# Kernel tuning notes

Hardware: AMD Instinct MI355X
Metric: run time of the kernel (lower is better)

Reference implementation:

```python
import jax, jax.numpy as jnp
import numpy as np

B, S, D = 8, 2048, 256
H = 4
DH = D // H  # 64


def setup_inputs() -> dict:
    key = jax.random.key(0)
    ks = jax.random.split(key, 6)
    x = jax.random.normal(ks[0], (B, S, D), dtype=jnp.float32)
    # Linear weights stored as (d_in, d_out) so y = x @ W (+ b)
    scale = 1.0 / np.sqrt(D)
    w_q = jax.random.normal(ks[1], (D, D), dtype=jnp.float32) * scale
    w_k = jax.random.normal(ks[2], (D, D), dtype=jnp.float32) * scale
    w_v = jax.random.normal(ks[3], (D, D), dtype=jnp.float32) * scale
    w_o = jax.random.normal(ks[4], (D, D), dtype=jnp.float32) * scale
    b_o = jax.random.normal(ks[5], (D,), dtype=jnp.float32) * 0.01
    return {"x": x, "w_q": w_q, "w_k": w_k, "w_v": w_v, "w_o": w_o, "b_o": b_o}


def reference(x, w_q, w_k, w_v, w_o, b_o):
    b, s, _ = x.shape
    # project and split heads: [b, h, s, dh]
    q = (x @ w_q).reshape(b, s, H, DH).transpose(0, 2, 1, 3)
    k = (x @ w_k).reshape(b, s, H, DH).transpose(0, 2, 1, 3)
    v = (x @ w_v).reshape(b, s, H, DH).transpose(0, 2, 1, 3)
    # full attention matrix [b, h, s, s] (matches original non-fused math)
    scores = jnp.einsum('bhqd,bhkd->bhqk', q, k) / jnp.sqrt(jnp.float32(DH))
    attn = jax.nn.softmax(scores, axis=-1)  # dropout is identity in eval
    ctx = jnp.einsum('bhqk,bhkd->bhqd', attn, v)
    ctx = ctx.transpose(0, 2, 1, 3).reshape(b, s, H * DH)
    return ctx @ w_o + b_o
```

## Files before the change

kernel.cpp:

```cpp
#include <hip/hip_runtime.h>
#include <hip/hip_fp16.h>
#include <math.h>

typedef _Float16 f16;
typedef _Float16 f16x8 __attribute__((ext_vector_type(8)));
typedef float f32x4 __attribute__((ext_vector_type(4)));

#define BB 8
#define SS 2048
#define DD 256
#define HH 4
#define DHH 64

#define LOG2E 1.44269504088896340736f
#define MOFF (4.0f * LOG2E)

__global__ __launch_bounds__(256) void prep_kernel(
    const float* __restrict__ wq, const float* __restrict__ wk,
    const float* __restrict__ wv, const float* __restrict__ wo,
    f16* __restrict__ wqkvT, f16* __restrict__ woT) {
  __shared__ f16 lds[64][72];
  int dout0 = blockIdx.x * 64;
  int k0 = blockIdx.y * 64;
  const float* src;
  f16* dst;
  int col0, drow;
  if (dout0 < 256)      { src = wq; dst = wqkvT; col0 = dout0;       drow = dout0; }
  else if (dout0 < 512) { src = wk; dst = wqkvT; col0 = dout0 - 256; drow = dout0; }
  else if (dout0 < 768) { src = wv; dst = wqkvT; col0 = dout0 - 512; drow = dout0; }
  else                  { src = wo; dst = woT;   col0 = dout0 - 768; drow = dout0 - 768; }

  int dl = threadIdx.x & 63, kl = threadIdx.x >> 6;
#pragma unroll
  for (int i = 0; i < 16; i++) {
    int kloc = i * 4 + kl;
    lds[kloc][dl] = (f16)src[(size_t)(k0 + kloc) * 256 + col0 + dl];
  }
  __syncthreads();
  int row_l = threadIdx.x >> 2, kq = threadIdx.x & 3;
  f16x8 v0, v1;
#pragma unroll
  for (int j = 0; j < 8; j++) v0[j] = lds[kq * 16 + j][row_l];
#pragma unroll
  for (int j = 0; j < 8; j++) v1[j] = lds[kq * 16 + 8 + j][row_l];
  f16* p = dst + (size_t)(drow + row_l) * 256 + k0 + kq * 16;
  *(f16x8*)p = v0;
  *(f16x8*)(p + 8) = v1;
}

__global__ __launch_bounds__(256) void qkv_gemm(
    const float* __restrict__ x, const f16* __restrict__ wT,
    f16* __restrict__ Q, f16* __restrict__ K, f16* __restrict__ VT) {
  __shared__ __attribute__((aligned(16))) f16 bstage[8][4][64][8];
  __shared__ __attribute__((aligned(16))) f16 lds_t[64][72];
  int m0 = blockIdx.x * 64;
  int which = blockIdx.y;
  int nbase = which * 256;
  int wave = threadIdx.x >> 6, lane = threadIdx.x & 63;
  int lm = lane & 15, quad = lane >> 4;

  const float* arow = x + (size_t)(m0 + wave * 16 + lm) * 256 + quad * 8;
  f16x8 a[8];
#pragma unroll
  for (int kk = 0; kk < 8; kk++) {
    f32x4 a0 = *(const f32x4*)(arow + kk * 32);
    f32x4 a1 = *(const f32x4*)(arow + kk * 32 + 4);
#pragma unroll
    for (int j = 0; j < 4; j++) { a[kk][j] = (f16)a0[j]; a[kk][j + 4] = (f16)a1[j]; }
  }

  f16x8 breg[8];
  auto bload = [&](int n0) {
#pragma unroll
    for (int kk = 0; kk < 8; kk++)
      breg[kk] = *(const f16x8*)(wT + (size_t)(n0 + wave * 16 + lm) * 256 + kk * 32 + quad * 8);
  };
  bload(nbase);

  int bb = m0 >> 11, s0 = m0 & 2047;
  for (int i = 0; i < 4; i++) {
    int n0 = nbase + i * 64;
#pragma unroll
    for (int kk = 0; kk < 8; kk++)
      *(f16x8*)&bstage[kk][wave][lane][0] = breg[kk];
    __syncthreads();
    if (i + 1 < 4) bload(nbase + (i + 1) * 64);

    f32x4 acc[4] = {};
#pragma unroll
    for (int kk = 0; kk < 8; kk++)
#pragma unroll
      for (int nt = 0; nt < 4; nt++) {
        f16x8 b = *(const f16x8*)&bstage[kk][nt][lane][0];
        acc[nt] = __builtin_amdgcn_mfma_f32_16x16x32_f16(a[kk], b, acc[nt], 0, 0, 0);
      }

    if (which < 2) {
      f16* dst = (which == 0) ? Q : K;
      int nb = n0 & 255;
#pragma unroll
      for (int nt = 0; nt < 4; nt++) {
        int dout = nb + nt * 16 + lm;
        int h = dout >> 6, dh = dout & 63;
#pragma unroll
        for (int r = 0; r < 4; r++) {
          int s = s0 + wave * 16 + quad * 4 + r;
          dst[(((size_t)(bb * HH + h) * SS + s) << 6) + dh] = (f16)acc[nt][r];
        }
      }
    } else {
      int h = i;
#pragma unroll
      for (int nt = 0; nt < 4; nt++)
#pragma unroll
        for (int r = 0; r < 4; r++)
          lds_t[nt * 16 + lm][wave * 16 + quad * 4 + r] = (f16)acc[nt][r];
      __syncthreads();
      int rr = threadIdx.x >> 2, cc = threadIdx.x & 3;
      f16* vrow = VT + ((size_t)(bb * HH + h) * DHH + rr) * SS + s0;
      f16x8 v0 = *(const f16x8*)&lds_t[rr][cc * 16];
      f16x8 v1 = *(const f16x8*)&lds_t[rr][cc * 16 + 8];
      *(f16x8*)(vrow + cc * 16) = v0;
      *(f16x8*)(vrow + cc * 16 + 8) = v1;
    }
    __syncthreads();
  }
}

__global__ __launch_bounds__(512) void attn_kernel(
    const f16* __restrict__ Q, const f16* __restrict__ K,
    const f16* __restrict__ VT, f16* __restrict__ ctx) {
  __shared__ __attribute__((aligned(16))) f16 kbuf[2][8][64][8];
  __shared__ __attribute__((aligned(16))) f16 vbuf[2][8][64][8];
  __shared__ __attribute__((aligned(16))) f16 lds_p[8][16][72];

  int qb = blockIdx.x, h = blockIdx.y, b = blockIdx.z;
  int wave = threadIdx.x >> 6, lane = threadIdx.x & 63;
  int lm = lane & 15, quad = lane >> 4;
  const f16* Qbh = Q + (size_t)(b * HH + h) * SS * DHH;
  const f16* Kbh = K + (size_t)(b * HH + h) * SS * DHH;
  const f16* Vbh = VT + (size_t)(b * HH + h) * DHH * SS;
  int q0 = qb * 128 + wave * 16;

  int kpf = wave >> 2, ntf = wave & 3;
  f16x8 tk, tv;
  auto stage_load = [&](int key0) {
    tk = *(const f16x8*)(Kbh + (key0 + ntf * 16 + lm) * DHH + kpf * 32 + quad * 8);
    tv = *(const f16x8*)(Vbh + (ntf * 16 + lm) * SS + key0 + kpf * 32 + quad * 8);
  };
  auto stage_write = [&](int buf) {
    *(f16x8*)&kbuf[buf][wave][lane][0] = tk;
    *(f16x8*)&vbuf[buf][wave][lane][0] = tv;
  };

  f16x8 aq[2];
#pragma unroll
  for (int kp = 0; kp < 2; kp++) {
    aq[kp] = *(const f16x8*)(Qbh + (q0 + lm) * DHH + kp * 32 + quad * 8);
#pragma unroll
    for (int j = 0; j < 8; j++) aq[kp][j] *= (f16)0.125f;
  }
  f16x8 vones;
#pragma unroll
  for (int j = 0; j < 8; j++) vones[j] = (f16)1.0f;

  f32x4 accO[4] = {};
  f32x4 accL = {};

  stage_load(0);
  stage_write(0);
  stage_load(64);

  const int NT = SS / 64;
  for (int t = 0; t < NT; t++) {
    int cur = t & 1;
    __syncthreads();

    if (t + 1 < NT) {
      stage_write(cur ^ 1);
      if (t + 2 < NT) stage_load((t + 2) * 64);
    }

    f32x4 accS[4] = {};
#pragma unroll
    for (int kp = 0; kp < 2; kp++)
#pragma unroll
      for (int nt = 0; nt < 4; nt++) {
        f16x8 bk = *(const f16x8*)&kbuf[cur][kp * 4 + nt][lane][0];
        accS[nt] = __builtin_amdgcn_mfma_f32_16x16x32_f16(aq[kp], bk, accS[nt], 0, 0, 0);
      }

#pragma unroll
    for (int nt = 0; nt < 4; nt++)
#pragma unroll
      for (int r = 0; r < 4; r++) {
        float p = __builtin_amdgcn_exp2f(__builtin_fmaf(accS[nt][r], LOG2E, -MOFF));
        lds_p[wave][quad * 4 + r][nt * 16 + lm] = (f16)p;
      }

#pragma unroll
    for (int kp = 0; kp < 2; kp++) {
      f16x8 ap = *(const f16x8*)&lds_p[wave][lm][kp * 32 + quad * 8];
      accL = __builtin_amdgcn_mfma_f32_16x16x32_f16(ap, vones, accL, 0, 0, 0);
#pragma unroll
      for (int nt = 0; nt < 4; nt++) {
        f16x8 bv = *(const f16x8*)&vbuf[cur][kp * 4 + nt][lane][0];
        accO[nt] = __builtin_amdgcn_mfma_f32_16x16x32_f16(ap, bv, accO[nt], 0, 0, 0);
      }
    }
  }

  float rinv[4];
#pragma unroll
  for (int r = 0; r < 4; r++) rinv[r] = 1.0f / accL[r];
#pragma unroll
  for (int nt = 0; nt < 4; nt++)
#pragma unroll
    for (int r = 0; r < 4; r++) {
      int s = q0 + quad * 4 + r;
      ctx[(size_t)(b * SS + s) * DD + h * DHH + nt * 16 + lm] =
          (f16)(accO[nt][r] * rinv[r]);
    }
}

__global__ __launch_bounds__(256) void out_gemm(
    const f16* __restrict__ ctxh, const f16* __restrict__ woT,
    const float* __restrict__ bo, float* __restrict__ out) {
  __shared__ __attribute__((aligned(16))) f16 bstage[8][4][64][8];
  int m0 = blockIdx.x * 64;
  int nbase = blockIdx.y * 128;
  int wave = threadIdx.x >> 6, lane = threadIdx.x & 63;
  int lm = lane & 15, quad = lane >> 4;
  const f16* arow = ctxh + (size_t)(m0 + wave * 16 + lm) * 256 + quad * 8;
  f16x8 a[8];
#pragma unroll
  for (int kk = 0; kk < 8; kk++) a[kk] = *(const f16x8*)(arow + kk * 32);

  f16x8 breg[8];
  auto bload = [&](int n0) {
#pragma unroll
    for (int kk = 0; kk < 8; kk++)
      breg[kk] = *(const f16x8*)(woT + (size_t)(n0 + wave * 16 + lm) * 256 + kk * 32 + quad * 8);
  };
  bload(nbase);

  for (int i = 0; i < 2; i++) {
    int n0 = nbase + i * 64;
#pragma unroll
    for (int kk = 0; kk < 8; kk++)
      *(f16x8*)&bstage[kk][wave][lane][0] = breg[kk];
    __syncthreads();
    if (i + 1 < 2) bload(nbase + 64);

    f32x4 acc[4] = {};
#pragma unroll
    for (int kk = 0; kk < 8; kk++)
#pragma unroll
      for (int nt = 0; nt < 4; nt++) {
        f16x8 bfr = *(const f16x8*)&bstage[kk][nt][lane][0];
        acc[nt] = __builtin_amdgcn_mfma_f32_16x16x32_f16(a[kk], bfr, acc[nt], 0, 0, 0);
      }
#pragma unroll
    for (int nt = 0; nt < 4; nt++) {
      int dout = n0 + nt * 16 + lm;
      float bias = bo[dout];
#pragma unroll
      for (int r = 0; r < 4; r++) {
        int t = m0 + wave * 16 + quad * 4 + r;
        out[(size_t)t * 256 + dout] = acc[nt][r] + bias;
      }
    }
    __syncthreads();
  }
}

extern "C" void kernel_launch(void* const* d_in, const int* in_sizes, int n_in,
                              void* d_out, int out_size, void* d_ws, size_t ws_size,
                              hipStream_t stream) {
  const float* x  = (const float*)d_in[0];
  const float* wq = (const float*)d_in[1];
  const float* wk = (const float*)d_in[2];
  const float* wv = (const float*)d_in[3];
  const float* wo = (const float*)d_in[4];
  const float* bo = (const float*)d_in[5];
  float* out = (float*)d_out;

  char* ws = (char*)d_ws;
  const size_t SZ = 8388608;
  f16* Qb    = (f16*)(ws);
  f16* Kb    = (f16*)(ws + SZ);
  f16* VTb   = (f16*)(ws + 2 * SZ);
  f16* ctxh  = (f16*)(ws + 3 * SZ);
  f16* wqkvT = (f16*)(ws + 4 * SZ);
  f16* woT   = (f16*)(ws + 4 * SZ + 393216);

  hipLaunchKernelGGL(prep_kernel, dim3(16, 4), dim3(256), 0, stream,
                     wq, wk, wv, wo, wqkvT, woT);
  hipLaunchKernelGGL(qkv_gemm, dim3(256, 3), dim3(256), 0, stream,
                     x, wqkvT, Qb, Kb, VTb);
  hipLaunchKernelGGL(attn_kernel, dim3(16, 4, 8), dim3(512), 0, stream,
                     Qb, Kb, VTb, ctxh);
  hipLaunchKernelGGL(out_gemm, dim3(256, 2), dim3(256), 0, stream,
                     ctxh, woT, bo, out);
}
```

Measured before the change: 160.6 us.

## Switch attention kernel to 32x32x16 MFMA with 32-row query tiles per wave

Rewrites the attention inner loop to use 32x32x16 f16 MFMA instructions. Each wave now owns 32 query rows, so a block has 4 waves (256 threads) covering the same 128 queries. Each thread stages two K and two V fragments per tile, and the P tile in LDS is reshaped to 32 rows. The larger MFMA shape should raise math per LDS read of K/V and cut the instruction count. In exchange it uses more accumulator registers per thread and has fewer waves per block to hide latency.

```diff
diff --git a/kernel.cpp b/kernel.cpp
--- a/kernel.cpp
+++ b/kernel.cpp
@@ -5,6 +5,7 @@
 typedef _Float16 f16;
 typedef _Float16 f16x8 __attribute__((ext_vector_type(8)));
 typedef float f32x4 __attribute__((ext_vector_type(4)));
+typedef float f32x16 __attribute__((ext_vector_type(16)));
 
 #define BB 8
 #define SS 2048
@@ -127,45 +128,49 @@
   }
 }
 
-__global__ __launch_bounds__(512) void attn_kernel(
+__global__ __launch_bounds__(256) void attn_kernel(
     const f16* __restrict__ Q, const f16* __restrict__ K,
     const f16* __restrict__ VT, f16* __restrict__ ctx) {
   __shared__ __attribute__((aligned(16))) f16 kbuf[2][8][64][8];
   __shared__ __attribute__((aligned(16))) f16 vbuf[2][8][64][8];
-  __shared__ __attribute__((aligned(16))) f16 lds_p[8][16][72];
+  __shared__ __attribute__((aligned(16))) f16 lds_p[4][32][72];
 
   int qb = blockIdx.x, h = blockIdx.y, b = blockIdx.z;
   int wave = threadIdx.x >> 6, lane = threadIdx.x & 63;
-  int lm = lane & 15, quad = lane >> 4;
+  int l31 = lane & 31, half = lane >> 5;
   const f16* Qbh = Q + (size_t)(b * HH + h) * SS * DHH;
   const f16* Kbh = K + (size_t)(b * HH + h) * SS * DHH;
   const f16* Vbh = VT + (size_t)(b * HH + h) * DHH * SS;
-  int q0 = qb * 128 + wave * 16;
-
-  int kpf = wave >> 2, ntf = wave & 3;
-  f16x8 tk, tv;
+  int q0 = qb * 128 + wave * 32;
+
+  int f0 = wave * 2, f1 = wave * 2 + 1;
+  f16x8 tk0, tk1, tv0, tv1;
   auto stage_load = [&](int key0) {
-    tk = *(const f16x8*)(Kbh + (key0 + ntf * 16 + lm) * DHH + kpf * 32 + quad * 8);
-    tv = *(const f16x8*)(Vbh + (ntf * 16 + lm) * SS + key0 + kpf * 32 + quad * 8);
+    tk0 = *(const f16x8*)(Kbh + (key0 + (f0 >> 2) * 32 + l31) * DHH + (f0 & 3) * 16 + half * 8);
+    tk1 = *(const f16x8*)(Kbh + (key0 + (f1 >> 2) * 32 + l31) * DHH + (f1 & 3) * 16 + half * 8);
+    tv0 = *(const f16x8*)(Vbh + ((f0 >> 2) * 32 + l31) * SS + key0 + (f0 & 3) * 16 + half * 8);
+    tv1 = *(const f16x8*)(Vbh + ((f1 >> 2) * 32 + l31) * SS + key0 + (f1 & 3) * 16 + half * 8);
   };
   auto stage_write = [&](int buf) {
-    *(f16x8*)&kbuf[buf][wave][lane][0] = tk;
-    *(f16x8*)&vbuf[buf][wave][lane][0] = tv;
+    *(f16x8*)&kbuf[buf][f0][lane][0] = tk0;
+    *(f16x8*)&kbuf[buf][f1][lane][0] = tk1;
+    *(f16x8*)&vbuf[buf][f0][lane][0] = tv0;
+    *(f16x8*)&vbuf[buf][f1][lane][0] = tv1;
   };
 
-  f16x8 aq[2];
-#pragma unroll
-  for (int kp = 0; kp < 2; kp++) {
-    aq[kp] = *(const f16x8*)(Qbh + (q0 + lm) * DHH + kp * 32 + quad * 8);
-#pragma unroll
-    for (int j = 0; j < 8; j++) aq[kp][j] *= (f16)0.125f;
+  f16x8 aq[4];
+#pragma unroll
+  for (int ks = 0; ks < 4; ks++) {
+    aq[ks] = *(const f16x8*)(Qbh + (q0 + l31) * DHH + ks * 16 + half * 8);
+#pragma unroll
+    for (int j = 0; j < 8; j++) aq[ks][j] *= (f16)0.125f;
   }
   f16x8 vones;
 #pragma unroll
   for (int j = 0; j < 8; j++) vones[j] = (f16)1.0f;
 
-  f32x4 accO[4] = {};
-  f32x4 accL = {};
+  f32x16 accO[2] = {};
+  f32x16 accL = {};
 
   stage_load(0);
   stage_write(0);
@@ -181,44 +186,46 @@
       if (t + 2 < NT) stage_load((t + 2) * 64);
     }
 
-    f32x4 accS[4] = {};
-#pragma unroll
-    for (int kp = 0; kp < 2; kp++)
-#pragma unroll
-      for (int nt = 0; nt < 4; nt++) {
-        f16x8 bk = *(const f16x8*)&kbuf[cur][kp * 4 + nt][lane][0];
-        accS[nt] = __builtin_amdgcn_mfma_f32_16x16x32_f16(aq[kp], bk, accS[nt], 0, 0, 0);
-      }
-
-#pragma unroll
-    for (int nt = 0; nt < 4; nt++)
-#pragma unroll
-      for (int r = 0; r < 4; r++) {
+    f32x16 accS[2] = {};
+#pragma unroll
+    for (int ks = 0; ks < 4; ks++)
+#pragma unroll
+      for (int nt = 0; nt < 2; nt++) {
+        f16x8 bk = *(const f16x8*)&kbuf[cur][nt * 4 + ks][lane][0];
+        accS[nt] = __builtin_amdgcn_mfma_f32_32x32x16_f16(aq[ks], bk, accS[nt], 0, 0, 0);
+      }
+
+#pragma unroll
+    for (int nt = 0; nt < 2; nt++)
+#pragma unroll
+      for (int r = 0; r < 16; r++) {
+        int row = (r & 3) + 8 * (r >> 2) + 4 * half;
         float p = __builtin_amdgcn_exp2f(__builtin_fmaf(accS[nt][r], LOG2E, -MOFF));
-        lds_p[wave][quad * 4 + r][nt * 16 + lm] = (f16)p;
-      }
-
-#pragma unroll
-    for (int kp = 0; kp < 2; kp++) {
-      f16x8 ap = *(const f16x8*)&lds_p[wave][lm][kp * 32 + quad * 8];
-      accL = __builtin_amdgcn_mfma_f32_16x16x32_f16(ap, vones, accL, 0, 0, 0);
-#pragma unroll
-      for (int nt = 0; nt < 4; nt++) {
-        f16x8 bv = *(const f16x8*)&vbuf[cur][kp * 4 + nt][lane][0];
-        accO[nt] = __builtin_amdgcn_mfma_f32_16x16x32_f16(ap, bv, accO[nt], 0, 0, 0);
-      }
-    }
-  }
-
-  float rinv[4];
-#pragma unroll
-  for (int r = 0; r < 4; r++) rinv[r] = 1.0f / accL[r];
-#pragma unroll
-  for (int nt = 0; nt < 4; nt++)
-#pragma unroll
-    for (int r = 0; r < 4; r++) {
-      int s = q0 + quad * 4 + r;
-      ctx[(size_t)(b * SS + s) * DD + h * DHH + nt * 16 + lm] =
+        lds_p[wave][row][nt * 32 + l31] = (f16)p;
+      }
+
+#pragma unroll
+    for (int ks = 0; ks < 4; ks++) {
+      f16x8 ap = *(const f16x8*)&lds_p[wave][l31][ks * 16 + half * 8];
+      accL = __builtin_amdgcn_mfma_f32_32x32x16_f16(ap, vones, accL, 0, 0, 0);
+#pragma unroll
+      for (int nt = 0; nt < 2; nt++) {
+        f16x8 bv = *(const f16x8*)&vbuf[cur][nt * 4 + ks][lane][0];
+        accO[nt] = __builtin_amdgcn_mfma_f32_32x32x16_f16(ap, bv, accO[nt], 0, 0, 0);
+      }
+    }
+  }
+
+  float rinv[16];
+#pragma unroll
+  for (int r = 0; r < 16; r++) rinv[r] = 1.0f / accL[r];
+#pragma unroll
+  for (int nt = 0; nt < 2; nt++)
+#pragma unroll
+    for (int r = 0; r < 16; r++) {
+      int row = (r & 3) + 8 * (r >> 2) + 4 * half;
+      int s = q0 + row;
+      ctx[(size_t)(b * SS + s) * DD + h * DHH + nt * 32 + l31] =
           (f16)(accO[nt][r] * rinv[r]);
     }
 }
@@ -298,7 +305,7 @@
                      wq, wk, wv, wo, wqkvT, woT);
   hipLaunchKernelGGL(qkv_gemm, dim3(256, 3), dim3(256), 0, stream,
                      x, wqkvT, Qb, Kb, VTb);
-  hipLaunchKernelGGL(attn_kernel, dim3(16, 4, 8), dim3(512), 0, stream,
+  hipLaunchKernelGGL(attn_kernel, dim3(16, 4, 8), dim3(256), 0, stream,
                      Qb, Kb, VTb, ctxh);
   hipLaunchKernelGGL(out_gemm, dim3(256, 2), dim3(256), 0, stream,
                      ctxh, woT, bo, out);
```

After: 165.5 us. 1.03x slower.
